# Optimization experiments

Measured on AMD Instinct MI355X. Metric: run time of the kernel, lower is better.

Reference implementation:

```python
import jax, jax.numpy as jnp
import numpy as np

DIM = 1024
NUM_HEADS = 16
HEAD_DIM = DIM // NUM_HEADS
SCALE = HEAD_DIM ** -0.5


def setup_inputs() -> dict:
    key = jax.random.key(0)
    ks = jax.random.split(key, 11)
    B, T = 2, 2048
    std = DIM ** -0.5
    return {
        "query": jax.random.normal(ks[0], (B, T, DIM), jnp.float32),
        "key": jax.random.normal(ks[1], (B, T, DIM), jnp.float32),
        "value": jax.random.normal(ks[2], (B, T, DIM), jnp.float32),
        "wq": jax.random.normal(ks[3], (DIM, DIM), jnp.float32) * std,
        "bq": jnp.zeros((DIM,), jnp.float32),
        "wk": jax.random.normal(ks[4], (DIM, DIM), jnp.float32) * std,
        "bk": jnp.zeros((DIM,), jnp.float32),
        "wv": jax.random.normal(ks[5], (DIM, DIM), jnp.float32) * std,
        "bv": jnp.zeros((DIM,), jnp.float32),
        "wo": jax.random.normal(ks[6], (DIM, DIM), jnp.float32) * std,
        "bo": jnp.zeros((DIM,), jnp.float32),
    }


def reference(query, key, value, wq, bq, wk, bk, wv, bv, wo, bo):
    B, Tq, D = query.shape
    Tk = key.shape[1]
    H, Hd = NUM_HEADS, HEAD_DIM
    # projections (torch Linear: x @ W^T + b); reshape to [B, H, T, Hd]
    q = (query @ wq.T + bq).reshape(B, Tq, H, Hd).transpose(0, 2, 1, 3)
    k = (key @ wk.T + bk).reshape(B, Tk, H, Hd).transpose(0, 2, 1, 3)
    v = (value @ wv.T + bv).reshape(B, Tk, H, Hd).transpose(0, 2, 1, 3)
    # attention scores [B, H, Tq, Tk]
    attn = jnp.einsum("bhqd,bhkd->bhqk", q, k) * SCALE
    attn = jax.nn.softmax(attn, axis=-1)
    # dropout p=0.0 -> identity
    out = jnp.einsum("bhqk,bhkd->bhqd", attn, v)
    out = out.transpose(0, 2, 1, 3).reshape(B, Tq, D)
    return out @ wo.T + bo
```

## Files before the change

### kernel.cpp

```cpp
#include <hip/hip_runtime.h>
#include <math.h>


typedef __attribute__((ext_vector_type(8))) short short8;
typedef __attribute__((ext_vector_type(4))) float f32x4;
typedef __attribute__((ext_vector_type(4))) float float4v;
typedef __attribute__((ext_vector_type(4))) unsigned short ushort4v;
typedef __attribute__((ext_vector_type(2))) unsigned int uint2v;

typedef __attribute__((address_space(3))) unsigned int lds_uint;
typedef __attribute__((address_space(1))) unsigned int glb_uint;

__device__ __forceinline__ void gload_lds16(const void* g, void* l) {
    __builtin_amdgcn_global_load_lds((glb_uint*)(unsigned long long)g,
                                     (lds_uint*)(unsigned int)(unsigned long long)l,
                                     16, 0, 0);
}

__device__ __forceinline__ unsigned short f32_bf16(float f) {
    union { float f; unsigned int u; } x; x.f = f;
    unsigned int r = x.u + 0x7fffu + ((x.u >> 16) & 1u);
    return (unsigned short)(r >> 16);
}

__device__ __forceinline__ unsigned int cvt_pk_bf16(float lo, float hi) {
    unsigned int r;
    asm("v_cvt_pk_bf16_f32 %0, %1, %2" : "=v"(r) : "v"(lo), "v"(hi));
    return r;
}

__device__ __forceinline__ float exp2_fast(float x) {
    float r;
    asm("v_exp_f32 %0, %1" : "=v"(r) : "v"(x));
    return r;
}

#define QSCALE 0.18033688011112042f

__global__ void pack3_bf16(const float* __restrict__ a, const float* __restrict__ b,
                           const float* __restrict__ c,
                           unsigned short* __restrict__ oa, unsigned short* __restrict__ ob,
                           unsigned short* __restrict__ oc, int n4) {
    const int y = blockIdx.y;
    const float* in = (y == 0) ? a : (y == 1) ? b : c;
    unsigned short* out = (y == 0) ? oa : (y == 1) ? ob : oc;
    int i = blockIdx.x * blockDim.x + threadIdx.x;
    if (i < n4) {
        float4v v = ((const float4v*)in)[i];
        ushort4v o;
        o.x = f32_bf16(v.x); o.y = f32_bf16(v.y);
        o.z = f32_bf16(v.z); o.w = f32_bf16(v.w);
        ((ushort4v*)out)[i] = o;
    }
}

__global__ void pack4_bf16(const float* __restrict__ a, const float* __restrict__ b,
                           const float* __restrict__ c, const float* __restrict__ d,
                           unsigned short* __restrict__ oa, unsigned short* __restrict__ ob,
                           unsigned short* __restrict__ oc, unsigned short* __restrict__ od,
                           int n4) {
    const int y = blockIdx.y;
    const float* in = (y == 0) ? a : (y == 1) ? b : (y == 2) ? c : d;
    unsigned short* out = (y == 0) ? oa : (y == 1) ? ob : (y == 2) ? oc : od;
    int i = blockIdx.x * blockDim.x + threadIdx.x;
    if (i < n4) {
        float4v v = ((const float4v*)in)[i];
        ushort4v o;
        o.x = f32_bf16(v.x); o.y = f32_bf16(v.y);
        o.z = f32_bf16(v.z); o.w = f32_bf16(v.w);
        ((ushort4v*)out)[i] = o;
    }
}

__global__ __launch_bounds__(256, 2) void gemm_qkv(
    const unsigned short* __restrict__ A0, const unsigned short* __restrict__ A1,
    const unsigned short* __restrict__ A2,
    const unsigned short* __restrict__ W0, const unsigned short* __restrict__ W1,
    const unsigned short* __restrict__ W2,
    const float* __restrict__ bs0, const float* __restrict__ bs1,
    const float* __restrict__ bs2,
    unsigned short* __restrict__ O0, unsigned short* __restrict__ O1,
    unsigned short* __restrict__ O2)
{
    const int z = blockIdx.z;
    const unsigned short* A = (z == 0) ? A0 : (z == 1) ? A1 : A2;
    const unsigned short* W = (z == 0) ? W0 : (z == 1) ? W1 : W2;
    const float* bias        = (z == 0) ? bs0 : (z == 1) ? bs1 : bs2;
    unsigned short* C        = (z == 0) ? O0 : (z == 1) ? O1 : O2;
    const float oscale = (z == 0) ? QSCALE : 1.0f;
    const int N = 1024, K = 1024;

    __shared__ unsigned short As[2][128 * 64];
    __shared__ unsigned short Bs[2][128 * 64];
    const int tid  = threadIdx.x;
    const int lane = tid & 63, wave = tid >> 6;
    const int l15 = lane & 15, l4 = lane >> 4;
    const int bm = blockIdx.y * 128, bn = blockIdx.x * 128;
    const int wr = wave >> 1, wc = wave & 1;

    f32x4 acc[4][4];
    #pragma unroll
    for (int i = 0; i < 4; ++i)
        #pragma unroll
        for (int j = 0; j < 4; ++j)
            #pragma unroll
            for (int e = 0; e < 4; ++e) acc[i][j][e] = 0.f;

    const int srow = lane >> 3;
    const int scol = (lane & 7) * 8;

    auto stage = [&](int bf, int k0) {
        #pragma unroll
        for (int i = 0; i < 4; ++i) {
            const int c = wave * 4 + i;
            const int row = c * 8 + srow;
            gload_lds16(A + (size_t)(bm + row) * K + k0 + scol, &As[bf][c * 512]);
            gload_lds16(W + (size_t)(bn + row) * K + k0 + scol, &Bs[bf][c * 512]);
        }
    };

    stage(0, 0);
    __syncthreads();

    int bufi = 0;
    for (int k0 = 0; k0 < K; k0 += 64) {
        if (k0 + 64 < K) stage(bufi ^ 1, k0 + 64);
        #pragma unroll
        for (int kk = 0; kk < 2; ++kk) {
            short8 af[4], bf[4];
            const int ko = kk * 32 + l4 * 8;
            #pragma unroll
            for (int i = 0; i < 4; ++i)
                af[i] = *(const short8*)&As[bufi][(wr * 64 + i * 16 + l15) * 64 + ko];
            #pragma unroll
            for (int j = 0; j < 4; ++j)
                bf[j] = *(const short8*)&Bs[bufi][(wc * 64 + j * 16 + l15) * 64 + ko];
            #pragma unroll
            for (int i = 0; i < 4; ++i)
                #pragma unroll
                for (int j = 0; j < 4; ++j)
                    acc[i][j] = __builtin_amdgcn_mfma_f32_16x16x32_bf16(
                        af[i], bf[j], acc[i][j], 0, 0, 0);
        }
        __syncthreads();
        bufi ^= 1;
    }

    #pragma unroll
    for (int j = 0; j < 4; ++j) {
        const int col = bn + wc * 64 + j * 16 + l15;
        const float bj = bias[col];
        #pragma unroll
        for (int i = 0; i < 4; ++i) {
            const int row0 = bm + wr * 64 + i * 16 + l4 * 4;
            #pragma unroll
            for (int r = 0; r < 4; ++r) {
                const int row = row0 + r;
                const float v = (acc[i][j][r] + bj) * oscale;
                if (z < 2) {
                    C[(size_t)row * N + col] = f32_bf16(v);
                } else {
                    const int b = row >> 11, t = row & 2047;
                    C[(((size_t)((b << 4) + (col >> 6)) * 64
                        + (col & 63)) << 11) + t] = f32_bf16(v);
                }
            }
        }
    }
}

__global__ __launch_bounds__(256, 3) void gemm_out(
    const unsigned short* __restrict__ A,
    const unsigned short* __restrict__ W,
    const float* __restrict__ bias,
    float* __restrict__ C)
{
    const int N = 1024, K = 1024;
    __shared__ unsigned short As[2][64 * 64];
    __shared__ unsigned short Bs[2][128 * 64];
    const int tid  = threadIdx.x;
    const int lane = tid & 63, wave = tid >> 6;
    const int l15 = lane & 15, l4 = lane >> 4;
    const int bm = blockIdx.y * 64, bn = blockIdx.x * 128;
    const int wr = wave >> 1, wc = wave & 1;

    f32x4 acc[2][4];
    #pragma unroll
    for (int i = 0; i < 2; ++i)
        #pragma unroll
        for (int j = 0; j < 4; ++j)
            #pragma unroll
            for (int e = 0; e < 4; ++e) acc[i][j][e] = 0.f;

    const int srow = lane >> 3;
    const int scol = (lane & 7) * 8;

    auto stage = [&](int bf, int k0) {
        #pragma unroll
        for (int i = 0; i < 2; ++i) {
            const int c = wave * 2 + i;
            gload_lds16(A + (size_t)(bm + c * 8 + srow) * K + k0 + scol,
                        &As[bf][c * 512]);
        }
        #pragma unroll
        for (int i = 0; i < 4; ++i) {
            const int c = wave * 4 + i;
            gload_lds16(W + (size_t)(bn + c * 8 + srow) * K + k0 + scol,
                        &Bs[bf][c * 512]);
        }
    };

    stage(0, 0);
    __syncthreads();

    int bufi = 0;
    for (int k0 = 0; k0 < K; k0 += 64) {
        if (k0 + 64 < K) stage(bufi ^ 1, k0 + 64);
        #pragma unroll
        for (int kk = 0; kk < 2; ++kk) {
            short8 af[2], bf[4];
            const int ko = kk * 32 + l4 * 8;
            #pragma unroll
            for (int i = 0; i < 2; ++i)
                af[i] = *(const short8*)&As[bufi][(wr * 32 + i * 16 + l15) * 64 + ko];
            #pragma unroll
            for (int j = 0; j < 4; ++j)
                bf[j] = *(const short8*)&Bs[bufi][(wc * 64 + j * 16 + l15) * 64 + ko];
            #pragma unroll
            for (int i = 0; i < 2; ++i)
                #pragma unroll
                for (int j = 0; j < 4; ++j)
                    acc[i][j] = __builtin_amdgcn_mfma_f32_16x16x32_bf16(
                        af[i], bf[j], acc[i][j], 0, 0, 0);
        }
        __syncthreads();
        bufi ^= 1;
    }

    #pragma unroll
    for (int j = 0; j < 4; ++j) {
        const int col = bn + wc * 64 + j * 16 + l15;
        const float bj = bias[col];
        #pragma unroll
        for (int i = 0; i < 2; ++i) {
            const int row0 = bm + wr * 32 + i * 16 + l4 * 4;
            #pragma unroll
            for (int r = 0; r < 4; ++r)
                C[(size_t)(row0 + r) * N + col] = acc[i][j][r] + bj;
        }
    }
}

__global__ __launch_bounds__(256, 4) void attn_fwd(
    const unsigned short* __restrict__ qp,
    const unsigned short* __restrict__ kp,
    const unsigned short* __restrict__ vt,
    unsigned short* __restrict__ op)
{
    __shared__ unsigned short Ks[2][64 * 64];
    __shared__ unsigned short Vs[2][64 * 64];
    __shared__ unsigned short P[4][16 * 64];

    const int tid = threadIdx.x;
    const int lane = tid & 63, wave = tid >> 6;
    const int l15 = lane & 15, l4 = lane >> 4;
    const int swz = (l15 & 7) << 3;

    const int flat = blockIdx.y * 32 + blockIdx.x;
    const int swzb = (flat & 7) * 128 + (flat >> 3);
    const int bx = swzb & 31;
    const int bh = swzb >> 5;
    const int b = bh >> 4, h = bh & 15;
    const int q0 = bx * 64 + wave * 16;

    const size_t xbase = (size_t)b * 2048 * 1024 + h * 64;
    const size_t vbase = (size_t)bh * 64 * 2048;

    const int sr = lane >> 3;
    const int sc = ((lane & 7) ^ sr) * 8;

    short8 bq[2];
    #pragma unroll
    for (int kk = 0; kk < 2; ++kk)
        bq[kk] = *(const short8*)&qp[xbase
            + (size_t)(q0 + l15) * 1024 + kk * 32 + l4 * 8];

    f32x4 acc[4];
    #pragma unroll
    for (int dj = 0; dj < 4; ++dj)
        #pragma unroll
        for (int e = 0; e < 4; ++e) acc[dj][e] = 0.f;

    float m_run = -1e30f, l_run = 0.f;

    {
        const int c0 = wave * 2;
        #pragma unroll
        for (int i = 0; i < 2; ++i) {
            const int c = c0 + i;
            gload_lds16(kp + xbase + (size_t)(c * 8 + sr) * 1024 + sc,
                        &Ks[0][c * 512]);
            gload_lds16(vt + vbase + (size_t)(c * 8 + sr) * 2048 + sc,
                        &Vs[0][c * 512]);
        }
    }
    __syncthreads();

    const int NT = 2048 / 64;
    int buf = 0;
    for (int t = 0; t < NT; ++t) {
        const int kv0 = t * 64;
        if (t + 1 < NT) {
            const int c0 = wave * 2;
            #pragma unroll
            for (int i = 0; i < 2; ++i) {
                const int c = c0 + i;
                gload_lds16(kp + xbase + (size_t)(kv0 + 64 + c * 8 + sr) * 1024 + sc,
                            &Ks[buf ^ 1][c * 512]);
                gload_lds16(vt + vbase + (size_t)(c * 8 + sr) * 2048 + kv0 + 64 + sc,
                            &Vs[buf ^ 1][c * 512]);
            }
        }

        f32x4 st[4];
        {
            short8 ak[4];
            #pragma unroll
            for (int j = 0; j < 4; ++j)
                ak[j] = *(const short8*)&Ks[buf][(j * 16 + l15) * 64
                                                 + (((0 * 4 + l4) << 3) ^ swz)];
            const f32x4 z4 = {0.f, 0.f, 0.f, 0.f};
            #pragma unroll
            for (int j = 0; j < 4; ++j)
                st[j] = __builtin_amdgcn_mfma_f32_16x16x32_bf16(
                    ak[j], bq[0], z4, 0, 0, 0);
            #pragma unroll
            for (int j = 0; j < 4; ++j)
                ak[j] = *(const short8*)&Ks[buf][(j * 16 + l15) * 64
                                                 + (((1 * 4 + l4) << 3) ^ swz)];
            #pragma unroll
            for (int j = 0; j < 4; ++j)
                st[j] = __builtin_amdgcn_mfma_f32_16x16x32_bf16(
                    ak[j], bq[1], st[j], 0, 0, 0);
        }

        short8 av[2][4];
        #pragma unroll
        for (int kvc = 0; kvc < 2; ++kvc)
            #pragma unroll
            for (int dj = 0; dj < 4; ++dj)
                av[kvc][dj] = *(const short8*)&Vs[buf][(dj * 16 + l15) * 64
                                                 + (((kvc * 4 + l4) << 3) ^ swz)];

        {
            float tm[4];
            #pragma unroll
            for (int j = 0; j < 4; ++j)
                tm[j] = fmaxf(fmaxf(st[j][0], st[j][1]),
                              fmaxf(st[j][2], st[j][3]));
            float mx = fmaxf(fmaxf(tm[0], tm[1]), fmaxf(tm[2], tm[3]));
            mx = fmaxf(mx, __shfl_xor(mx, 16));
            mx = fmaxf(mx, __shfl_xor(mx, 32));
            const float mnew = fmaxf(m_run, mx);
            const float corr = exp2_fast(m_run - mnew);
            m_run = mnew;
            float ts[4];
            #pragma unroll
            for (int j = 0; j < 4; ++j) {
                float p0 = exp2_fast(st[j][0] - mnew);
                float p1 = exp2_fast(st[j][1] - mnew);
                float p2 = exp2_fast(st[j][2] - mnew);
                float p3 = exp2_fast(st[j][3] - mnew);
                st[j][0] = p0; st[j][1] = p1; st[j][2] = p2; st[j][3] = p3;
                ts[j] = (p0 + p1) + (p2 + p3);
            }
            float ls = (ts[0] + ts[1]) + (ts[2] + ts[3]);
            ls += __shfl_xor(ls, 16);
            ls += __shfl_xor(ls, 32);
            l_run = l_run * corr + ls;
            #pragma unroll
            for (int dj = 0; dj < 4; ++dj) acc[dj] *= corr;
        }

        #pragma unroll
        for (int j = 0; j < 4; ++j) {
            uint2v w;
            w.x = cvt_pk_bf16(st[j][0], st[j][1]);
            w.y = cvt_pk_bf16(st[j][2], st[j][3]);
            *(uint2v*)&P[wave][l15 * 64 + ((j * 16 + l4 * 4) ^ swz)] = w;
        }

        #pragma unroll
        for (int kvc = 0; kvc < 2; ++kvc) {
            short8 pb = *(const short8*)&P[wave][l15 * 64
                                                + (((kvc * 4 + l4) << 3) ^ swz)];
            #pragma unroll
            for (int dj = 0; dj < 4; ++dj)
                acc[dj] = __builtin_amdgcn_mfma_f32_16x16x32_bf16(
                    av[kvc][dj], pb, acc[dj], 0, 0, 0);
        }

        __syncthreads();
        buf ^= 1;
    }

    {
        const float inv = 1.0f / l_run;
        const int t = q0 + l15;
        #pragma unroll
        for (int dj = 0; dj < 4; ++dj) {
            uint2v w;
            w.x = cvt_pk_bf16(acc[dj][0] * inv, acc[dj][1] * inv);
            w.y = cvt_pk_bf16(acc[dj][2] * inv, acc[dj][3] * inv);
            *(uint2v*)&op[((size_t)(b * 2048 + t)) * 1024
                          + h * 64 + dj * 16 + l4 * 4] = w;
        }
    }
}

extern "C" void kernel_launch(void* const* d_in, const int* in_sizes, int n_in,
                              void* d_out, int out_size, void* d_ws, size_t ws_size,
                              hipStream_t stream)
{
    const float* q  = (const float*)d_in[0];
    const float* k  = (const float*)d_in[1];
    const float* v  = (const float*)d_in[2];
    const float* wq = (const float*)d_in[3];
    const float* bq = (const float*)d_in[4];
    const float* wk = (const float*)d_in[5];
    const float* bk = (const float*)d_in[6];
    const float* wv = (const float*)d_in[7];
    const float* bv = (const float*)d_in[8];
    const float* wo = (const float*)d_in[9];
    const float* bo = (const float*)d_in[10];
    float* out = (float*)d_out;

    const int M = 4096, N = 1024, K = 1024;
    unsigned char* ws = (unsigned char*)d_ws;
    const size_t SX = (size_t)M * K * 2;
    const size_t SW = (size_t)N * K * 2;
    unsigned short* xq  = (unsigned short*)(ws);
    unsigned short* xk  = (unsigned short*)(ws + SX);
    unsigned short* xv  = (unsigned short*)(ws + 2 * SX);
    unsigned short* wqb = (unsigned short*)(ws + 3 * SX);
    unsigned short* wkb = (unsigned short*)(ws + 3 * SX + SW);
    unsigned short* wvb = (unsigned short*)(ws + 3 * SX + 2 * SW);
    unsigned short* wob = (unsigned short*)(ws + 3 * SX + 3 * SW);
    unsigned short* qp  = (unsigned short*)(ws + 3 * SX + 4 * SW);
    unsigned short* kp  = qp + (size_t)M * N;
    unsigned short* vt  = kp + (size_t)M * N;
    unsigned short* opb = vt + (size_t)M * N;

    pack3_bf16<<<dim3(4096, 3), 256, 0, stream>>>(q, k, v, xq, xk, xv,
                                                  M * K / 4);
    pack4_bf16<<<dim3(1024, 4), 256, 0, stream>>>(wq, wk, wv, wo,
                                                  wqb, wkb, wvb, wob, N * K / 4);

    gemm_qkv<<<dim3(8, 32, 3), 256, 0, stream>>>(xq, xk, xv, wqb, wkb, wvb,
                                                 bq, bk, bv, qp, kp, vt);

    attn_fwd<<<dim3(32, 32), 256, 0, stream>>>(qp, kp, vt, opb);

    gemm_out<<<dim3(8, 64), 256, 0, stream>>>(opb, wob, bo, out);
}
```

Baseline: 152.7 us.

## Software-pipeline attention QK with softmax, single-buffer the QKV GEMM

The attention kernel's KV loop is unrolled by two with ping-pong LDS buffers. The next tile's QK^T MFMAs are issued before the current tile's softmax and PV, so matrix work can overlap the exp/reduction work, and s_setprio is raised around the MFMA bursts. The QKV projection GEMM drops its double-buffered LDS prefetch for a single buffer with load-then-sync, which halves its LDS footprint but no longer overlaps global loads with MFMAs. The attention change adds sync points and register pressure, and the GEMM change may expose load latency.

```diff
diff --git a/kernel.cpp b/kernel.cpp
--- a/kernel.cpp
+++ b/kernel.cpp
@@ -90,8 +90,8 @@
     const float oscale = (z == 0) ? QSCALE : 1.0f;
     const int N = 1024, K = 1024;
 
-    __shared__ unsigned short As[2][128 * 64];
-    __shared__ unsigned short Bs[2][128 * 64];
+    __shared__ unsigned short As[128 * 64];
+    __shared__ unsigned short Bs[128 * 64];
     const int tid  = threadIdx.x;
     const int lane = tid & 63, wave = tid >> 6;
     const int l15 = lane & 15, l4 = lane >> 4;
@@ -109,32 +109,26 @@
     const int srow = lane >> 3;
     const int scol = (lane & 7) * 8;
 
-    auto stage = [&](int bf, int k0) {
+    for (int k0 = 0; k0 < K; k0 += 64) {
+        __syncthreads();
         #pragma unroll
         for (int i = 0; i < 4; ++i) {
-            const int c = wave * 4 + i;
-            const int row = c * 8 + srow;
-            gload_lds16(A + (size_t)(bm + row) * K + k0 + scol, &As[bf][c * 512]);
-            gload_lds16(W + (size_t)(bn + row) * K + k0 + scol, &Bs[bf][c * 512]);
-        }
-    };
-
-    stage(0, 0);
-    __syncthreads();
-
-    int bufi = 0;
-    for (int k0 = 0; k0 < K; k0 += 64) {
-        if (k0 + 64 < K) stage(bufi ^ 1, k0 + 64);
+            int c = wave * 4 + i;
+            int row = c * 8 + srow;
+            gload_lds16(A + (size_t)(bm + row) * K + k0 + scol, &As[c * 512]);
+            gload_lds16(W + (size_t)(bn + row) * K + k0 + scol, &Bs[c * 512]);
+        }
+        __syncthreads();
         #pragma unroll
         for (int kk = 0; kk < 2; ++kk) {
             short8 af[4], bf[4];
             const int ko = kk * 32 + l4 * 8;
             #pragma unroll
             for (int i = 0; i < 4; ++i)
-                af[i] = *(const short8*)&As[bufi][(wr * 64 + i * 16 + l15) * 64 + ko];
+                af[i] = *(const short8*)&As[(wr * 64 + i * 16 + l15) * 64 + ko];
             #pragma unroll
             for (int j = 0; j < 4; ++j)
-                bf[j] = *(const short8*)&Bs[bufi][(wc * 64 + j * 16 + l15) * 64 + ko];
+                bf[j] = *(const short8*)&Bs[(wc * 64 + j * 16 + l15) * 64 + ko];
             #pragma unroll
             for (int i = 0; i < 4; ++i)
                 #pragma unroll
@@ -142,8 +136,6 @@
                     acc[i][j] = __builtin_amdgcn_mfma_f32_16x16x32_bf16(
                         af[i], bf[j], acc[i][j], 0, 0, 0);
         }
-        __syncthreads();
-        bufi ^= 1;
     }
 
     #pragma unroll
@@ -293,94 +285,80 @@
 
     float m_run = -1e30f, l_run = 0.f;
 
-    {
+    auto stage = [&](int bf, int kv) {
         const int c0 = wave * 2;
         #pragma unroll
         for (int i = 0; i < 2; ++i) {
             const int c = c0 + i;
-            gload_lds16(kp + xbase + (size_t)(c * 8 + sr) * 1024 + sc,
-                        &Ks[0][c * 512]);
-            gload_lds16(vt + vbase + (size_t)(c * 8 + sr) * 2048 + sc,
-                        &Vs[0][c * 512]);
-        }
-    }
-    __syncthreads();
-
-    const int NT = 2048 / 64;
-    int buf = 0;
-    for (int t = 0; t < NT; ++t) {
-        const int kv0 = t * 64;
-        if (t + 1 < NT) {
-            const int c0 = wave * 2;
-            #pragma unroll
-            for (int i = 0; i < 2; ++i) {
-                const int c = c0 + i;
-                gload_lds16(kp + xbase + (size_t)(kv0 + 64 + c * 8 + sr) * 1024 + sc,
-                            &Ks[buf ^ 1][c * 512]);
-                gload_lds16(vt + vbase + (size_t)(c * 8 + sr) * 2048 + kv0 + 64 + sc,
-                            &Vs[buf ^ 1][c * 512]);
-            }
-        }
-
-        f32x4 st[4];
-        {
-            short8 ak[4];
-            #pragma unroll
-            for (int j = 0; j < 4; ++j)
-                ak[j] = *(const short8*)&Ks[buf][(j * 16 + l15) * 64
-                                                 + (((0 * 4 + l4) << 3) ^ swz)];
-            const f32x4 z4 = {0.f, 0.f, 0.f, 0.f};
-            #pragma unroll
-            for (int j = 0; j < 4; ++j)
-                st[j] = __builtin_amdgcn_mfma_f32_16x16x32_bf16(
-                    ak[j], bq[0], z4, 0, 0, 0);
-            #pragma unroll
-            for (int j = 0; j < 4; ++j)
-                ak[j] = *(const short8*)&Ks[buf][(j * 16 + l15) * 64
-                                                 + (((1 * 4 + l4) << 3) ^ swz)];
-            #pragma unroll
-            for (int j = 0; j < 4; ++j)
-                st[j] = __builtin_amdgcn_mfma_f32_16x16x32_bf16(
-                    ak[j], bq[1], st[j], 0, 0, 0);
-        }
-
-        short8 av[2][4];
+            gload_lds16(kp + xbase + (size_t)(kv + c * 8 + sr) * 1024 + sc,
+                        &Ks[bf][c * 512]);
+            gload_lds16(vt + vbase + (size_t)(c * 8 + sr) * 2048 + kv + sc,
+                        &Vs[bf][c * 512]);
+        }
+    };
+
+    auto qk = [&](int bf, f32x4* st) {
+        short8 ak[4];
+        #pragma unroll
+        for (int j = 0; j < 4; ++j)
+            ak[j] = *(const short8*)&Ks[bf][(j * 16 + l15) * 64
+                                            + ((l4 << 3) ^ swz)];
+        const f32x4 z4 = {0.f, 0.f, 0.f, 0.f};
+        __builtin_amdgcn_s_setprio(1);
+        #pragma unroll
+        for (int j = 0; j < 4; ++j)
+            st[j] = __builtin_amdgcn_mfma_f32_16x16x32_bf16(
+                ak[j], bq[0], z4, 0, 0, 0);
+        __builtin_amdgcn_s_setprio(0);
+        #pragma unroll
+        for (int j = 0; j < 4; ++j)
+            ak[j] = *(const short8*)&Ks[bf][(j * 16 + l15) * 64
+                                            + (((4 + l4) << 3) ^ swz)];
+        __builtin_amdgcn_s_setprio(1);
+        #pragma unroll
+        for (int j = 0; j < 4; ++j)
+            st[j] = __builtin_amdgcn_mfma_f32_16x16x32_bf16(
+                ak[j], bq[1], st[j], 0, 0, 0);
+        __builtin_amdgcn_s_setprio(0);
+    };
+
+    auto avr = [&](int bf, short8 (*av)[4]) {
         #pragma unroll
         for (int kvc = 0; kvc < 2; ++kvc)
             #pragma unroll
             for (int dj = 0; dj < 4; ++dj)
-                av[kvc][dj] = *(const short8*)&Vs[buf][(dj * 16 + l15) * 64
-                                                 + (((kvc * 4 + l4) << 3) ^ swz)];
-
-        {
-            float tm[4];
-            #pragma unroll
-            for (int j = 0; j < 4; ++j)
-                tm[j] = fmaxf(fmaxf(st[j][0], st[j][1]),
-                              fmaxf(st[j][2], st[j][3]));
-            float mx = fmaxf(fmaxf(tm[0], tm[1]), fmaxf(tm[2], tm[3]));
-            mx = fmaxf(mx, __shfl_xor(mx, 16));
-            mx = fmaxf(mx, __shfl_xor(mx, 32));
-            const float mnew = fmaxf(m_run, mx);
-            const float corr = exp2_fast(m_run - mnew);
-            m_run = mnew;
-            float ts[4];
-            #pragma unroll
-            for (int j = 0; j < 4; ++j) {
-                float p0 = exp2_fast(st[j][0] - mnew);
-                float p1 = exp2_fast(st[j][1] - mnew);
-                float p2 = exp2_fast(st[j][2] - mnew);
-                float p3 = exp2_fast(st[j][3] - mnew);
-                st[j][0] = p0; st[j][1] = p1; st[j][2] = p2; st[j][3] = p3;
-                ts[j] = (p0 + p1) + (p2 + p3);
-            }
-            float ls = (ts[0] + ts[1]) + (ts[2] + ts[3]);
-            ls += __shfl_xor(ls, 16);
-            ls += __shfl_xor(ls, 32);
-            l_run = l_run * corr + ls;
-            #pragma unroll
-            for (int dj = 0; dj < 4; ++dj) acc[dj] *= corr;
-        }
+                av[kvc][dj] = *(const short8*)&Vs[bf][(dj * 16 + l15) * 64
+                                                + (((kvc * 4 + l4) << 3) ^ swz)];
+    };
+
+    auto smpv = [&](f32x4* st, short8 (*av)[4]) {
+        float tm[4];
+        #pragma unroll
+        for (int j = 0; j < 4; ++j)
+            tm[j] = fmaxf(fmaxf(st[j][0], st[j][1]),
+                          fmaxf(st[j][2], st[j][3]));
+        float mx = fmaxf(fmaxf(tm[0], tm[1]), fmaxf(tm[2], tm[3]));
+        mx = fmaxf(mx, __shfl_xor(mx, 16));
+        mx = fmaxf(mx, __shfl_xor(mx, 32));
+        const float mnew = fmaxf(m_run, mx);
+        const float corr = exp2_fast(m_run - mnew);
+        m_run = mnew;
+        float ts[4];
+        #pragma unroll
+        for (int j = 0; j < 4; ++j) {
+            float p0 = exp2_fast(st[j][0] - mnew);
+            float p1 = exp2_fast(st[j][1] - mnew);
+            float p2 = exp2_fast(st[j][2] - mnew);
+            float p3 = exp2_fast(st[j][3] - mnew);
+            st[j][0] = p0; st[j][1] = p1; st[j][2] = p2; st[j][3] = p3;
+            ts[j] = (p0 + p1) + (p2 + p3);
+        }
+        float ls = (ts[0] + ts[1]) + (ts[2] + ts[3]);
+        ls += __shfl_xor(ls, 16);
+        ls += __shfl_xor(ls, 32);
+        l_run = l_run * corr + ls;
+        #pragma unroll
+        for (int dj = 0; dj < 4; ++dj) acc[dj] *= corr;
 
         #pragma unroll
         for (int j = 0; j < 4; ++j) {
@@ -394,14 +372,36 @@
         for (int kvc = 0; kvc < 2; ++kvc) {
             short8 pb = *(const short8*)&P[wave][l15 * 64
                                                 + (((kvc * 4 + l4) << 3) ^ swz)];
+            __builtin_amdgcn_s_setprio(1);
             #pragma unroll
             for (int dj = 0; dj < 4; ++dj)
                 acc[dj] = __builtin_amdgcn_mfma_f32_16x16x32_bf16(
                     av[kvc][dj], pb, acc[dj], 0, 0, 0);
-        }
-
-        __syncthreads();
-        buf ^= 1;
+            __builtin_amdgcn_s_setprio(0);
+        }
+    };
+
+    stage(0, 0);
+    __syncthreads();
+    stage(1, 64);
+    f32x4 stA[4], stB[4];
+    qk(0, stA);
+    short8 av[2][4];
+
+    const int NT = 32;
+    for (int t = 0; t < NT; t += 2) {
+        avr(0, av);
+        __syncthreads();
+        if (t + 2 < NT) stage(0, (t + 2) << 6);
+        if (t + 1 < NT) qk(1, stB);
+        smpv(stA, av);
+        __syncthreads();
+        avr(1, av);
+        __syncthreads();
+        if (t + 3 < NT) stage(1, (t + 3) << 6);
+        if (t + 2 < NT) qk(0, stA);
+        smpv(stB, av);
+        __syncthreads();
     }
 
     {
```

Result: slower. 184.1 us (+20.5%).
